# Performance work log

Hardware: AMD Instinct MI355X
Metric: run time of the kernel (lower is better)

## Reference

```python
import jax, jax.numpy as jnp
import numpy as np

B, T, C = 4, 2048, 1024
N_HEAD = 16
HEAD_DIM = C // N_HEAD


def setup_inputs() -> dict:
    key = jax.random.key(0)
    ks = jax.random.split(key, 5)
    bound = 1.0 / np.sqrt(C)
    x = jax.random.normal(ks[0], (B, T, C), dtype=jnp.float32)
    W_attn = jax.random.uniform(ks[1], (C, 3 * C), minval=-bound, maxval=bound, dtype=jnp.float32)
    b_attn = jax.random.uniform(ks[2], (3 * C,), minval=-bound, maxval=bound, dtype=jnp.float32)
    W_proj = jax.random.uniform(ks[3], (C, C), minval=-bound, maxval=bound, dtype=jnp.float32)
    b_proj = jax.random.uniform(ks[4], (C,), minval=-bound, maxval=bound, dtype=jnp.float32)
    return {"x": x, "W_attn": W_attn, "b_attn": b_attn, "W_proj": W_proj, "b_proj": b_proj}


def reference(x, W_attn, b_attn, W_proj, b_proj):
    Bx, Tx, Cx = x.shape
    qkv = x @ W_attn + b_attn                       # [B,T,3C]
    q, k, v = jnp.split(qkv, 3, axis=2)
    # [B,T,C] -> [B,H,T,D]
    q = q.reshape(Bx, Tx, N_HEAD, HEAD_DIM).transpose(0, 2, 1, 3)
    k = k.reshape(Bx, Tx, N_HEAD, HEAD_DIM).transpose(0, 2, 1, 3)
    v = v.reshape(Bx, Tx, N_HEAD, HEAD_DIM).transpose(0, 2, 1, 3)
    scale = 1.0 / np.sqrt(HEAD_DIM).astype(np.float32)
    att = jnp.einsum('bhqd,bhkd->bhqk', q, k) * scale   # [B,H,T,T]
    causal = jnp.tril(jnp.ones((Tx, Tx), dtype=bool))
    att = jnp.where(causal[None, None], att, -jnp.inf)
    att = jax.nn.softmax(att, axis=-1)
    y = jnp.einsum('bhqk,bhkd->bhqd', att, v)           # [B,H,T,D]
    y = y.transpose(0, 2, 1, 3).reshape(Bx, Tx, Cx)
    return y @ W_proj + b_proj
```

## Files before the change

kernel.cpp:

```cpp
#include <hip/hip_runtime.h>

#define Bsz 4
#define Tn 2048
#define Cn 1024
#define Hn 16
#define Dn 64
#define Mn (Bsz * Tn)
#define NQKV (3 * Cn)
#define BH (Bsz * Hn)

typedef short bf16x8_t __attribute__((ext_vector_type(8)));
typedef float f32x4 __attribute__((ext_vector_type(4)));

static __device__ __forceinline__ float exp2_fast(float x) {
    return __builtin_amdgcn_exp2f(x);
}

static __device__ __forceinline__ unsigned short f2bf(float f) {
    union { float f; unsigned int u; } v; v.f = f;
    unsigned int r = v.u + 0x7FFFu + ((v.u >> 16) & 1u);
    return (unsigned short)(r >> 16);
}

static __device__ __forceinline__ unsigned int fbits(float f) {
    union { float f; unsigned int u; } v; v.f = f; return v.u;
}

static __device__ __forceinline__ bf16x8_t ld_frag(const unsigned short* p) {
    bf16x8_t r;
    *reinterpret_cast<float4*>(&r) = *reinterpret_cast<const float4*>(p);
    return r;
}

#define ASYNC_COPY16(gp, lp)                                                         \
    __builtin_amdgcn_global_load_lds((__attribute__((address_space(1))) void*)(gp),  \
                                     (__attribute__((address_space(3))) void*)(lp),  \
                                     16, 0, 0)

__global__ void cast_f32_bf16(const float* __restrict__ src,
                              unsigned short* __restrict__ dst, int n4) {
    int i = blockIdx.x * blockDim.x + threadIdx.x;
    if (i < n4) {
        float4 v = reinterpret_cast<const float4*>(src)[i];
        ushort4 o;
        o.x = f2bf(v.x); o.y = f2bf(v.y); o.z = f2bf(v.z); o.w = f2bf(v.w);
        reinterpret_cast<ushort4*>(dst)[i] = o;
    }
}

__global__ void transpose_cast(const float* __restrict__ src,
                               unsigned short* __restrict__ dst, int R, int Cc) {
    __shared__ float tile[32][33];
    int c0 = blockIdx.x * 32, r0 = blockIdx.y * 32;
    int tx = threadIdx.x & 31, ty = threadIdx.x >> 5;
#pragma unroll
    for (int i = 0; i < 4; i++)
        tile[ty + i * 8][tx] = src[(long)(r0 + ty + i * 8) * Cc + c0 + tx];
    __syncthreads();
#pragma unroll
    for (int i = 0; i < 4; i++)
        dst[(long)(c0 + ty + i * 8) * R + r0 + tx] = f2bf(tile[tx][ty + i * 8]);
}

template <int MODE>
__global__ __launch_bounds__(256) void gemm128(const unsigned short* __restrict__ A,
                                               const unsigned short* __restrict__ Bt,
                                               const float* __restrict__ bias,
                                               float* __restrict__ outF,
                                               unsigned short* __restrict__ Qb,
                                               unsigned short* __restrict__ Kb,
                                               unsigned short* __restrict__ Vt,
                                               int M, int N, int Kd) {
    __shared__ __align__(16) unsigned short As[128 * 32];
    __shared__ __align__(16) unsigned short Bs[128 * 32];
    int n0 = blockIdx.x * 128, m0 = blockIdx.y * 128;
    int tid = threadIdx.x;
    int lane = tid & 63, w = tid >> 6;
    int wm = w >> 1, wn = w & 1;
    int quad = lane >> 4, l15 = lane & 15;
    int r = lane >> 2, c = lane & 3;

    const unsigned short* AgBase = A + (long)(m0 + w * 32 + r) * Kd + c * 8;
    const unsigned short* BgBase = Bt + (long)(n0 + w * 32 + r) * Kd + c * 8;
    unsigned short* ldsA = As + (w * 32) * 32;
    unsigned short* ldsB = Bs + (w * 32) * 32;

    f32x4 acc[4][4] = {};

    for (int kb = 0; kb < Kd; kb += 32) {
        ASYNC_COPY16(AgBase + kb, ldsA);
        ASYNC_COPY16(AgBase + 16 * Kd + kb, ldsA + 512);
        ASYNC_COPY16(BgBase + kb, ldsB);
        ASYNC_COPY16(BgBase + 16 * Kd + kb, ldsB + 512);
        __syncthreads();
        bf16x8_t af[4], bfr[4];
#pragma unroll
        for (int i = 0; i < 4; i++)
            af[i] = ld_frag(&As[(wm * 64 + i * 16 + l15) * 32 + quad * 8]);
#pragma unroll
        for (int j = 0; j < 4; j++)
            bfr[j] = ld_frag(&Bs[(wn * 64 + j * 16 + l15) * 32 + quad * 8]);
#pragma unroll
        for (int i = 0; i < 4; i++)
#pragma unroll
            for (int j = 0; j < 4; j++)
                acc[i][j] = __builtin_amdgcn_mfma_f32_16x16x32_bf16(af[i], bfr[j], acc[i][j], 0, 0, 0);
        __syncthreads();
    }

#pragma unroll
    for (int i = 0; i < 4; i++)
#pragma unroll
        for (int j = 0; j < 4; j++) {
            int col = n0 + wn * 64 + j * 16 + l15;
            float bval = bias[col];
#pragma unroll
            for (int rr = 0; rr < 4; rr++) {
                int row = m0 + wm * 64 + i * 16 + quad * 4 + rr;
                float val = acc[i][j][rr] + bval;
                if (MODE == 0) {
                    outF[(long)row * N + col] = val;
                } else {
                    int seg = col >> 10, within = col & 1023;
                    int h = within >> 6, d = within & 63;
                    int b = row >> 11, t = row & 2047;
                    int bh = b * Hn + h;
                    if (seg == 0) {
                        Qb[((long)bh * Tn + t) * Dn + d] = f2bf(val * 0.18033688f);
                    } else if (seg == 1) {
                        Kb[((long)bh * Tn + t) * Dn + d] = f2bf(val);
                    } else {
                        Vt[((long)bh * Dn + d) * Tn + t] = f2bf(val);
                    }
                }
            }
        }
}

__global__ __launch_bounds__(256) void attn_kernel(const unsigned short* __restrict__ Qb,
                                                   const unsigned short* __restrict__ Kb,
                                                   const unsigned short* __restrict__ Vt,
                                                   unsigned short* __restrict__ Yb) {
    __shared__ __align__(16) unsigned short Ks[64 * 72];
    __shared__ __align__(16) unsigned short Vs[64 * 72];
    __shared__ __align__(16) unsigned short Plds[4][2][16 * 72];
    int tid = threadIdx.x, w = tid >> 6, lane = tid & 63;
    int quad = lane >> 4, l15 = lane & 15;

    int flat = blockIdx.y * 8 + blockIdx.x;
    int xcd = flat & 7, slot = flat >> 3;
    int bh = xcd * 8 + (slot >> 3);
    int qx = slot & 7;
    int b = bh >> 4, h = bh & 15;

    const unsigned short* Qh = Qb + (long)bh * Tn * Dn;
    const unsigned short* Kh = Kb + (long)bh * Tn * Dn;
    const unsigned short* Vh = Vt + (long)bh * Dn * Tn;

    int sr = tid >> 3;
    int sc = (tid & 7) * 8;

#pragma unroll 1
    for (int s = 0; s < 2; s++) {
        int qi = s ? (15 - qx) : qx;
        int q0b = qi * 128;
        int nt = 2 * qi + 2;

        bf16x8_t qf[2][2];
#pragma unroll
        for (int h2 = 0; h2 < 2; h2++) {
            int qrow = q0b + h2 * 64 + w * 16 + l15;
            qf[h2][0] = ld_frag(&Qh[qrow * Dn + quad * 8]);
            qf[h2][1] = ld_frag(&Qh[qrow * Dn + 32 + quad * 8]);
        }

        float l_acc[2] = {0.f, 0.f};
        f32x4 Of[2][4] = {};

        float4 kr0 = *reinterpret_cast<const float4*>(&Kh[sr * Dn + sc]);
        float4 kr1 = *reinterpret_cast<const float4*>(&Kh[(32 + sr) * Dn + sc]);
        float4 vr0 = *reinterpret_cast<const float4*>(&Vh[sr * Tn + sc]);
        float4 vr1 = *reinterpret_cast<const float4*>(&Vh[(32 + sr) * Tn + sc]);

#pragma unroll 1
        for (int t = 0; t < nt; t++) {
            int kt0 = t * 64;
            __syncthreads();
            *reinterpret_cast<float4*>(&Ks[sr * 72 + sc]) = kr0;
            *reinterpret_cast<float4*>(&Ks[(32 + sr) * 72 + sc]) = kr1;
            *reinterpret_cast<float4*>(&Vs[sr * 72 + sc]) = vr0;
            *reinterpret_cast<float4*>(&Vs[(32 + sr) * 72 + sc]) = vr1;
            if (t + 1 < nt) {
                int kn = kt0 + 64;
                kr0 = *reinterpret_cast<const float4*>(&Kh[(kn + sr) * Dn + sc]);
                kr1 = *reinterpret_cast<const float4*>(&Kh[(kn + 32 + sr) * Dn + sc]);
                vr0 = *reinterpret_cast<const float4*>(&Vh[sr * Tn + kn + sc]);
                vr1 = *reinterpret_cast<const float4*>(&Vh[(32 + sr) * Tn + kn + sc]);
            }
            __syncthreads();

            bool act0 = (kt0 <= q0b);

            f32x4 st[2][4];
            __builtin_amdgcn_s_setprio(1);
#pragma unroll
            for (int ti = 0; ti < 4; ti++) {
                bf16x8_t ka0 = ld_frag(&Ks[(ti * 16 + l15) * 72 + quad * 8]);
                bf16x8_t ka1 = ld_frag(&Ks[(ti * 16 + l15) * 72 + 32 + quad * 8]);
                if (act0) {
                    f32x4 z = {};
                    z = __builtin_amdgcn_mfma_f32_16x16x32_bf16(ka0, qf[0][0], z, 0, 0, 0);
                    st[0][ti] = __builtin_amdgcn_mfma_f32_16x16x32_bf16(ka1, qf[0][1], z, 0, 0, 0);
                }
                f32x4 z1 = {};
                z1 = __builtin_amdgcn_mfma_f32_16x16x32_bf16(ka0, qf[1][0], z1, 0, 0, 0);
                st[1][ti] = __builtin_amdgcn_mfma_f32_16x16x32_bf16(ka1, qf[1][1], z1, 0, 0, 0);
            }
            __builtin_amdgcn_s_setprio(0);

            bf16x8_t pa[2][2];
#pragma unroll
            for (int h2 = 0; h2 < 2; h2++) {
                int qbase = q0b + h2 * 64;
                if (h2 == 0 && !act0) continue;
                if (kt0 == qbase) {
                    int q_glob = qbase + w * 16 + l15;
#pragma unroll
                    for (int ti = 0; ti < 4; ti++)
#pragma unroll
                        for (int rr = 0; rr < 4; rr++)
                            if (kt0 + ti * 16 + quad * 4 + rr > q_glob) st[h2][ti][rr] = -1e30f;
                }
                float lsum = 0.f;
#pragma unroll
                for (int ti = 0; ti < 4; ti++)
#pragma unroll
                    for (int rr = 0; rr < 4; rr++) {
                        float e = exp2_fast(st[h2][ti][rr]);
                        st[h2][ti][rr] = e;
                        lsum += e;
                    }
                l_acc[h2] += lsum;
                unsigned short* Pw = &Plds[w][h2][0];
#pragma unroll
                for (int ti = 0; ti < 4; ti++) {
                    unsigned u0 = fbits(st[h2][ti][0]) + 0x8000u;
                    unsigned u1 = fbits(st[h2][ti][1]) + 0x8000u;
                    unsigned u2 = fbits(st[h2][ti][2]) + 0x8000u;
                    unsigned u3 = fbits(st[h2][ti][3]) + 0x8000u;
                    uint2 pk;
                    pk.x = __builtin_amdgcn_perm(u1, u0, 0x07060302);
                    pk.y = __builtin_amdgcn_perm(u3, u2, 0x07060302);
                    *reinterpret_cast<uint2*>(&Pw[l15 * 72 + ti * 16 + quad * 4]) = pk;
                }
#pragma unroll
                for (int kc = 0; kc < 2; kc++)
                    pa[h2][kc] = ld_frag(&Pw[l15 * 72 + kc * 32 + quad * 8]);
            }

            __builtin_amdgcn_s_setprio(1);
#pragma unroll
            for (int kc = 0; kc < 2; kc++)
#pragma unroll
                for (int dt = 0; dt < 4; dt++) {
                    bf16x8_t vb = ld_frag(&Vs[(dt * 16 + l15) * 72 + kc * 32 + quad * 8]);
                    if (act0)
                        Of[0][dt] = __builtin_amdgcn_mfma_f32_16x16x32_bf16(pa[0][kc], vb, Of[0][dt], 0, 0, 0);
                    Of[1][dt] = __builtin_amdgcn_mfma_f32_16x16x32_bf16(pa[1][kc], vb, Of[1][dt], 0, 0, 0);
                }
            __builtin_amdgcn_s_setprio(0);
        }

#pragma unroll
        for (int h2 = 0; h2 < 2; h2++) {
            float l_tot = l_acc[h2];
            l_tot += __shfl_xor(l_tot, 16);
            l_tot += __shfl_xor(l_tot, 32);
            int qw = q0b + h2 * 64 + w * 16;
#pragma unroll
            for (int rr = 0; rr < 4; rr++) {
                float linv = 1.f / __shfl(l_tot, quad * 4 + rr);
                int t = qw + quad * 4 + rr;
                long rowbase = ((long)(b * Tn + t)) * Cn + h * Dn;
#pragma unroll
                for (int dt = 0; dt < 4; dt++)
                    Yb[rowbase + dt * 16 + l15] = f2bf(Of[h2][dt][rr] * linv);
            }
        }
    }
}

extern "C" void kernel_launch(void* const* d_in, const int* in_sizes, int n_in,
                              void* d_out, int out_size, void* d_ws, size_t ws_size,
                              hipStream_t stream) {
    const float* x      = (const float*)d_in[0];
    const float* W_attn = (const float*)d_in[1];
    const float* b_attn = (const float*)d_in[2];
    const float* W_proj = (const float*)d_in[3];
    const float* b_proj = (const float*)d_in[4];
    float* out = (float*)d_out;

    unsigned short* xb      = (unsigned short*)d_ws;
    unsigned short* Wqkv_t  = xb + (size_t)Mn * Cn;
    unsigned short* Wproj_t = Wqkv_t + (size_t)NQKV * Cn;
    unsigned short* Qb      = Wproj_t + (size_t)Cn * Cn;
    unsigned short* Kb      = Qb + (size_t)BH * Tn * Dn;
    unsigned short* Vt      = Kb + (size_t)BH * Tn * Dn;
    unsigned short* Yb      = Vt + (size_t)BH * Tn * Dn;

    cast_f32_bf16<<<(Mn * Cn / 4 + 255) / 256, 256, 0, stream>>>(x, xb, Mn * Cn / 4);
    transpose_cast<<<dim3(NQKV / 32, Cn / 32), 256, 0, stream>>>(W_attn, Wqkv_t, Cn, NQKV);
    transpose_cast<<<dim3(Cn / 32, Cn / 32), 256, 0, stream>>>(W_proj, Wproj_t, Cn, Cn);

    gemm128<1><<<dim3(NQKV / 128, Mn / 128), 256, 0, stream>>>(
        xb, Wqkv_t, b_attn, nullptr, Qb, Kb, Vt, Mn, NQKV, Cn);

    attn_kernel<<<dim3(8, BH), 256, 0, stream>>>(Qb, Kb, Vt, Yb);

    gemm128<0><<<dim3(Cn / 128, Mn / 128), 256, 0, stream>>>(
        Yb, Wproj_t, b_proj, out, nullptr, nullptr, nullptr, Mn, Cn, Cn);
}
```

Before: 283.0 us.

## Load K/V MFMA fragments directly from global memory, dropping LDS staging

The attention kernel no longer stages K and V tiles through shared memory behind two block barriers per tile. Each wave now loads its own K and V fragments straight from global memory into registers. This removes the __syncthreads and LDS traffic, but all four waves now fetch the same K/V data redundantly, relying on L1/L2 caching, and the software prefetch of the next tile is gone, so load latency is exposed.

```diff
diff --git a/kernel.cpp b/kernel.cpp
--- a/kernel.cpp
+++ b/kernel.cpp
@@ -36,6 +36,8 @@
     __builtin_amdgcn_global_load_lds((__attribute__((address_space(1))) void*)(gp),  \
                                      (__attribute__((address_space(3))) void*)(lp),  \
                                      16, 0, 0)
+
+#define MFMA_B16(a, b, c) __builtin_amdgcn_mfma_f32_16x16x32_bf16(a, b, c, 0, 0, 0)
 
 __global__ void cast_f32_bf16(const float* __restrict__ src,
                               unsigned short* __restrict__ dst, int n4) {
@@ -141,8 +143,6 @@
                                                    const unsigned short* __restrict__ Kb,
                                                    const unsigned short* __restrict__ Vt,
                                                    unsigned short* __restrict__ Yb) {
-    __shared__ __align__(16) unsigned short Ks[64 * 72];
-    __shared__ __align__(16) unsigned short Vs[64 * 72];
     __shared__ __align__(16) unsigned short Plds[4][2][16 * 72];
     int tid = threadIdx.x, w = tid >> 6, lane = tid & 63;
     int quad = lane >> 4, l15 = lane & 15;
@@ -157,9 +157,6 @@
     const unsigned short* Kh = Kb + (long)bh * Tn * Dn;
     const unsigned short* Vh = Vt + (long)bh * Dn * Tn;
 
-    int sr = tid >> 3;
-    int sc = (tid & 7) * 8;
-
 #pragma unroll 1
     for (int s = 0; s < 2; s++) {
         int qi = s ? (15 - qx) : qx;
@@ -177,46 +174,41 @@
         float l_acc[2] = {0.f, 0.f};
         f32x4 Of[2][4] = {};
 
-        float4 kr0 = *reinterpret_cast<const float4*>(&Kh[sr * Dn + sc]);
-        float4 kr1 = *reinterpret_cast<const float4*>(&Kh[(32 + sr) * Dn + sc]);
-        float4 vr0 = *reinterpret_cast<const float4*>(&Vh[sr * Tn + sc]);
-        float4 vr1 = *reinterpret_cast<const float4*>(&Vh[(32 + sr) * Tn + sc]);
-
 #pragma unroll 1
         for (int t = 0; t < nt; t++) {
             int kt0 = t * 64;
-            __syncthreads();
-            *reinterpret_cast<float4*>(&Ks[sr * 72 + sc]) = kr0;
-            *reinterpret_cast<float4*>(&Ks[(32 + sr) * 72 + sc]) = kr1;
-            *reinterpret_cast<float4*>(&Vs[sr * 72 + sc]) = vr0;
-            *reinterpret_cast<float4*>(&Vs[(32 + sr) * 72 + sc]) = vr1;
-            if (t + 1 < nt) {
-                int kn = kt0 + 64;
-                kr0 = *reinterpret_cast<const float4*>(&Kh[(kn + sr) * Dn + sc]);
-                kr1 = *reinterpret_cast<const float4*>(&Kh[(kn + 32 + sr) * Dn + sc]);
-                vr0 = *reinterpret_cast<const float4*>(&Vh[sr * Tn + kn + sc]);
-                vr1 = *reinterpret_cast<const float4*>(&Vh[(32 + sr) * Tn + kn + sc]);
-            }
-            __syncthreads();
-
             bool act0 = (kt0 <= q0b);
+
+            bf16x8_t kf0[4], kf1[4];
+#pragma unroll
+            for (int ti = 0; ti < 4; ti++) {
+                const unsigned short* kp = &Kh[(kt0 + ti * 16 + l15) * Dn + quad * 8];
+                kf0[ti] = ld_frag(kp);
+                kf1[ti] = ld_frag(kp + 32);
+            }
 
             f32x4 st[2][4];
             __builtin_amdgcn_s_setprio(1);
 #pragma unroll
             for (int ti = 0; ti < 4; ti++) {
-                bf16x8_t ka0 = ld_frag(&Ks[(ti * 16 + l15) * 72 + quad * 8]);
-                bf16x8_t ka1 = ld_frag(&Ks[(ti * 16 + l15) * 72 + 32 + quad * 8]);
                 if (act0) {
                     f32x4 z = {};
-                    z = __builtin_amdgcn_mfma_f32_16x16x32_bf16(ka0, qf[0][0], z, 0, 0, 0);
-                    st[0][ti] = __builtin_amdgcn_mfma_f32_16x16x32_bf16(ka1, qf[0][1], z, 0, 0, 0);
+                    z = __builtin_amdgcn_mfma_f32_16x16x32_bf16(kf0[ti], qf[0][0], z, 0, 0, 0);
+                    st[0][ti] = __builtin_amdgcn_mfma_f32_16x16x32_bf16(kf1[ti], qf[0][1], z, 0, 0, 0);
                 }
                 f32x4 z1 = {};
-                z1 = __builtin_amdgcn_mfma_f32_16x16x32_bf16(ka0, qf[1][0], z1, 0, 0, 0);
-                st[1][ti] = __builtin_amdgcn_mfma_f32_16x16x32_bf16(ka1, qf[1][1], z1, 0, 0, 0);
+                z1 = __builtin_amdgcn_mfma_f32_16x16x32_bf16(kf0[ti], qf[1][0], z1, 0, 0, 0);
+                st[1][ti] = __builtin_amdgcn_mfma_f32_16x16x32_bf16(kf1[ti], qf[1][1], z1, 0, 0, 0);
             }
             __builtin_amdgcn_s_setprio(0);
+
+            bf16x8_t vf[4][2];
+#pragma unroll
+            for (int dt = 0; dt < 4; dt++) {
+                const unsigned short* vp = &Vh[(long)(dt * 16 + l15) * Tn + kt0 + quad * 8];
+                vf[dt][0] = ld_frag(vp);
+                vf[dt][1] = ld_frag(vp + 32);
+            }
 
             bf16x8_t pa[2][2];
 #pragma unroll
@@ -263,10 +255,9 @@
             for (int kc = 0; kc < 2; kc++)
 #pragma unroll
                 for (int dt = 0; dt < 4; dt++) {
-                    bf16x8_t vb = ld_frag(&Vs[(dt * 16 + l15) * 72 + kc * 32 + quad * 8]);
                     if (act0)
-                        Of[0][dt] = __builtin_amdgcn_mfma_f32_16x16x32_bf16(pa[0][kc], vb, Of[0][dt], 0, 0, 0);
-                    Of[1][dt] = __builtin_amdgcn_mfma_f32_16x16x32_bf16(pa[1][kc], vb, Of[1][dt], 0, 0, 0);
+                        Of[0][dt] = __builtin_amdgcn_mfma_f32_16x16x32_bf16(pa[0][kc], vf[dt][kc], Of[0][dt], 0, 0, 0);
+                    Of[1][dt] = __builtin_amdgcn_mfma_f32_16x16x32_bf16(pa[1][kc], vf[dt][kc], Of[1][dt], 0, 0, 0);
                 }
             __builtin_amdgcn_s_setprio(0);
         }
```

Result: slower. 343.3 us (+21.3%).
